# Kernel tuning notes

Hardware: AMD Instinct MI355X
Metric: run time of the kernel (lower is better)

## Reference

```python
import jax, jax.numpy as jnp
import numpy as np

SIGMA = 0.03   # self.sig = [0.03] in the original module
EPS = 1e-12    # guard for degenerate (zero-area) faces from random indices


def _mesh_quantities(V, F):
    """Face centers, areas (|0.5*cross|) and unit normals. V:[Nv,3], F:[Nf,3] int."""
    v0 = V[F[:, 0]]
    v1 = V[F[:, 1]]
    v2 = V[F[:, 2]]
    C = (v0 + v1 + v2) / 3.0                      # [Nf,3] face centers
    N = 0.5 * jnp.cross(v1 - v0, v2 - v0)         # [Nf,3] area-weighted normals
    L = jnp.linalg.norm(N, axis=-1)               # [Nf]  face areas
    Nn = N / jnp.maximum(L, EPS)[:, None]         # [Nf,3] unit normals
    return C, L, Nn


def _kernel_sum(Cx, Lx, Nx, Cy, Ly, Ny, gamma):
    """sum_ij Lx_i Ly_j exp(-gamma |Cx_i-Cy_j|^2) <Nx_i,Ny_j>^2  (unoriented Gauss-squared varifold kernel)."""
    d2 = (jnp.sum(Cx * Cx, -1)[:, None]
          + jnp.sum(Cy * Cy, -1)[None, :]
          - 2.0 * Cx @ Cy.T)                       # [F,F]
    dot = Nx @ Ny.T                                # [F,F]
    K = jnp.exp(-gamma * d2) * (dot * dot)
    return jnp.einsum('i,ij,j->', Lx, K, Ly)


def reference(predictions, targets, faces):
    gamma = 1.0 / (SIGMA * SIGMA)

    def per_sample(carry, xy):
        Vs, Vt = xy
        Cs, Ls, Ns = _mesh_quantities(Vs, faces)
        Ct, Lt, Nt = _mesh_quantities(Vt, faces)
        li = (_kernel_sum(Cs, Ls, Ns, Cs, Ls, Ns, gamma)
              + _kernel_sum(Ct, Lt, Nt, Ct, Lt, Nt, gamma)
              - 2.0 * _kernel_sum(Cs, Ls, Ns, Ct, Lt, Nt, gamma))
        return carry + li, None

    total, _ = jax.lax.scan(per_sample,
                            jnp.asarray(0.0, predictions.dtype),
                            (predictions, targets))
    return (total / predictions.shape[0])[None]   # shape [1], like torch.Tensor([0.0])


def setup_inputs() -> dict:
    key = jax.random.key(0)
    k1, k2, k3 = jax.random.split(key, 3)
    B, NV, NF = 4, 5023, 9976
    # scale 0.02 so inter-face distances are commensurate with sigma=0.03
    predictions = 0.02 * jax.random.normal(k1, (B, NV, 3), dtype=jnp.float32)
    targets = 0.02 * jax.random.normal(k2, (B, NV, 3), dtype=jnp.float32)
    faces = jax.random.randint(k3, (NF, 3), 0, NV, dtype=jnp.int32)
    return {"predictions": predictions, "targets": targets, "faces": faces}
```

## Files before the change

kernel.cpp:

```cpp
#include <hip/hip_runtime.h>


#define NVERT 5023
#define NFACE 9976
#define BATCH 4
#define HALFP 9984
#define NTP   (2 * HALFP)
#define NTOT  (BATCH * NTP)
#define NCH   624
#define NPAN  78
#define SPLITS 26

constexpr float GAMMA = 1.0f / (0.03f * 0.03f);
constexpr float LOG2E = 1.4426950408889634f;
constexpr float EPSV  = 1e-12f;

typedef _Float16 half8_t  __attribute__((ext_vector_type(8)));
typedef float    f32x16   __attribute__((ext_vector_type(16)));
typedef float    f32x2    __attribute__((ext_vector_type(2)));

__global__ __launch_bounds__(256)
void face_quant_kernel(const float* __restrict__ pred,
                       const float* __restrict__ targ,
                       const int*   __restrict__ faces,
                       _Float16*    __restrict__ fd,
                       float*       __restrict__ out) {
    int idx = blockIdx.x * 256 + threadIdx.x;
    if (idx == 0) out[0] = 0.0f;
    if (idx >= NTOT) return;

    int b     = idx / NTP;
    int s     = idx - b * NTP;
    int which = (s >= HALFP) ? 1 : 0;
    int f     = s - which * HALFP;

    _Float16* arec = fd + (size_t)idx * 32;
    _Float16* brec = fd + (size_t)NTOT * 32 + (size_t)idx * 32;

    if (f >= NFACE) {
        half8_t z = {};
        *(half8_t*)(arec + 0) = z; *(half8_t*)(arec + 8)  = z;
        *(half8_t*)(arec + 16) = z; *(half8_t*)(arec + 24) = z;
        *(half8_t*)(brec + 0) = z; *(half8_t*)(brec + 8)  = z;
        *(half8_t*)(brec + 16) = z; *(half8_t*)(brec + 24) = z;
        return;
    }

    const float* V = (which ? targ : pred) + (size_t)b * NVERT * 3;
    int i0 = faces[f * 3 + 0];
    int i1 = faces[f * 3 + 1];
    int i2 = faces[f * 3 + 2];

    float v0x = V[i0*3+0], v0y = V[i0*3+1], v0z = V[i0*3+2];
    float v1x = V[i1*3+0], v1y = V[i1*3+1], v1z = V[i1*3+2];
    float v2x = V[i2*3+0], v2y = V[i2*3+1], v2z = V[i2*3+2];

    const float third = 1.0f / 3.0f;
    float cx = (v0x + v1x + v2x) * third;
    float cy = (v0y + v1y + v2y) * third;
    float cz = (v0z + v1z + v2z) * third;

    float e1x = v1x - v0x, e1y = v1y - v0y, e1z = v1z - v0z;
    float e2x = v2x - v0x, e2y = v2y - v0y, e2z = v2z - v0z;

    float nx = 0.5f * (e1y * e2z - e1z * e2y);
    float ny = 0.5f * (e1z * e2x - e1x * e2z);
    float nz = 0.5f * (e1x * e2y - e1y * e2x);

    float L   = sqrtf(nx*nx + ny*ny + nz*nz);
    float inv = 1.0f / fmaxf(L, EPSV);
    float sc  = inv * sqrtf(L);
    float mx = nx * sc, my = ny * sc, mz = nz * sc;

    const float TG = 2.0f * GAMMA * LOG2E;
    float tgx = TG * cx, tgy = TG * cy, tgz = TG * cz;
    float cq  = -GAMMA * LOG2E * (cx*cx + cy*cy + cz*cz);

    _Float16 TGxh = (_Float16)tgx; _Float16 TGxl = (_Float16)(tgx - (float)TGxh);
    _Float16 TGyh = (_Float16)tgy; _Float16 TGyl = (_Float16)(tgy - (float)TGyh);
    _Float16 TGzh = (_Float16)tgz; _Float16 TGzl = (_Float16)(tgz - (float)TGzh);
    _Float16 Cxh  = (_Float16)cx;  _Float16 Cxl  = (_Float16)(cx  - (float)Cxh);
    _Float16 Cyh  = (_Float16)cy;  _Float16 Cyl  = (_Float16)(cy  - (float)Cyh);
    _Float16 Czh  = (_Float16)cz;  _Float16 Czl  = (_Float16)(cz  - (float)Czh);
    _Float16 cqh  = (_Float16)cq;  _Float16 cql  = (_Float16)(cq  - (float)cqh);
    _Float16 mxh  = (_Float16)mx;  _Float16 mxl  = (_Float16)(mx  - (float)mxh);
    _Float16 myh  = (_Float16)my;  _Float16 myl  = (_Float16)(my  - (float)myh);
    _Float16 mzh  = (_Float16)mz;  _Float16 mzl  = (_Float16)(mz  - (float)mzh);
    _Float16 one  = (_Float16)1.0f;
    _Float16 zz   = (_Float16)0.0f;

    half8_t ta0 = {TGxh, TGyh, TGzh, TGxl, TGyl, TGzl, TGxh, TGyh};
    half8_t ta1 = {TGzh, TGxl, TGyl, TGzl, cqh,  cql,  one,  one };
    half8_t da0 = {mxh,  myh,  mzh,  mxl,  myl,  mzl,  mxh,  myh };
    half8_t da1 = {mzh,  mxl,  myl,  mzl,  zz,   zz,   zz,   zz  };
    half8_t tb0 = {Cxh,  Cyh,  Czh,  Cxh,  Cyh,  Czh,  Cxl,  Cyl };
    half8_t tb1 = {Czl,  Cxl,  Cyl,  Czl,  one,  one,  cqh,  cql };
    half8_t db0 = {mxh,  myh,  mzh,  mxh,  myh,  mzh,  mxl,  myl };
    half8_t db1 = {mzl,  mxl,  myl,  mzl,  zz,   zz,   zz,   zz  };

    *(half8_t*)(arec + 0)  = ta0;  *(half8_t*)(arec + 8)  = ta1;
    *(half8_t*)(arec + 16) = da0;  *(half8_t*)(arec + 24) = da1;
    *(half8_t*)(brec + 0)  = tb0;  *(half8_t*)(brec + 8)  = tb1;
    *(half8_t*)(brec + 16) = db0;  *(half8_t*)(brec + 24) = db1;
}

__device__ __forceinline__ half8_t ld8(const _Float16* p) {
    return *(const half8_t*)p;
}

__global__ __launch_bounds__(256, 4)
void pair_sum_kernel(const _Float16* __restrict__ fd,
                     float*          __restrict__ out) {
    const int b       = blockIdx.z;
    const int pairIdx = blockIdx.x / SPLITS;
    const int s       = blockIdx.x % SPLITS;

    const _Float16* Arec = fd;
    const _Float16* Brec = fd + (size_t)NTOT * 32;

    const int lane = threadIdx.x & 63;
    const int w    = threadIdx.x >> 6;
    const int col  = lane & 31;
    const int koff = (lane >> 5) * 8;

    const size_t bface = (size_t)b * NTP;
    const size_t JSTEP = (size_t)SPLITS * 32 * 32;

    float acc = 0.0f;

    #pragma unroll 1
    for (int h = 0; h < 2; ++h) {
        const int   P  = h ? (NPAN - 1 - pairIdx) : pairIdx;
        const int   c0 = 8 * P;
        const float si = (P < NPAN / 2) ? 1.0f : -1.0f;
        const int   iters = (NCH - c0 - s + SPLITS - 1) / SPLITS;
        if (iters <= 0) continue;

        const _Float16* ap0 = Arec + (bface + (size_t)(P * 256 + w * 32 + col)) * 32 + koff;
        const _Float16* ap1 = ap0 + (size_t)128 * 32;
        half8_t aT0 = ld8(ap0);
        half8_t aD0 = ld8(ap0 + 16);
        half8_t aT1 = ld8(ap1);
        half8_t aD1 = ld8(ap1 + 16);

        const _Float16* pB = Brec + (bface + (size_t)((c0 + s) * 32 + col)) * 32 + koff;
        half8_t bT = ld8(pB);
        half8_t bD = ld8(pB + 16);

        f32x16 z = {};

        #pragma unroll 1
        for (int k = 0; k < iters; ++k) {
            const _Float16* pN = (k + 1 < iters) ? (pB + JSTEP) : pB;
            half8_t nT = ld8(pN);
            half8_t nD = ld8(pN + 16);
            pB = pN;

            f32x16 T0 = __builtin_amdgcn_mfma_f32_32x32x16_f16(aT0, bT, z, 0, 0, 0);
            f32x16 D0 = __builtin_amdgcn_mfma_f32_32x32x16_f16(aD0, bD, z, 0, 0, 0);
            f32x16 T1 = __builtin_amdgcn_mfma_f32_32x32x16_f16(aT1, bT, z, 0, 0, 0);
            f32x16 D1 = __builtin_amdgcn_mfma_f32_32x32x16_f16(aD1, bD, z, 0, 0, 0);

            f32x2 ts0 = {0.f, 0.f}, ts1 = {0.f, 0.f};
            #pragma unroll
            for (int r = 0; r < 16; r += 2) {
                f32x2 e0 = {__builtin_amdgcn_exp2f(T0[r]),
                            __builtin_amdgcn_exp2f(T0[r + 1])};
                f32x2 d0 = {D0[r], D0[r + 1]};
                d0 = d0 * d0;
                ts0 = e0 * d0 + ts0;
                f32x2 e1 = {__builtin_amdgcn_exp2f(T1[r]),
                            __builtin_amdgcn_exp2f(T1[r + 1])};
                f32x2 d1 = {D1[r], D1[r + 1]};
                d1 = d1 * d1;
                ts1 = e1 * d1 + ts1;
            }

            const int   jc  = c0 + s + SPLITS * k;
            const float sj  = (jc < NCH / 2) ? si : -si;
            const float wgt = (k == 0 && s < 8) ? 1.0f : 2.0f;
            acc = fmaf(sj * wgt, ts0.x + ts0.y + ts1.x + ts1.y, acc);

            bT = nT; bD = nD;
        }
    }

    acc *= (1.0f / BATCH);

    #pragma unroll
    for (int off = 32; off > 0; off >>= 1)
        acc += __shfl_down(acc, off, 64);

    __shared__ float wsum[4];
    if (lane == 0) wsum[w] = acc;
    __syncthreads();
    if (threadIdx.x == 0)
        atomicAdd(out, wsum[0] + wsum[1] + wsum[2] + wsum[3]);
}

extern "C" void kernel_launch(void* const* d_in, const int* in_sizes, int n_in,
                              void* d_out, int out_size, void* d_ws, size_t ws_size,
                              hipStream_t stream) {
    const float* pred  = (const float*)d_in[0];
    const float* targ  = (const float*)d_in[1];
    const int*   faces = (const int*)d_in[2];
    float*       out   = (float*)d_out;
    _Float16*    fd    = (_Float16*)d_ws;

    face_quant_kernel<<<(NTOT + 255) / 256, 256, 0, stream>>>(
        pred, targ, faces, fd, out);

    dim3 grid((NPAN / 2) * SPLITS, 1, BATCH);
    pair_sum_kernel<<<grid, 256, 0, stream>>>(fd, out);
}
```

Before: 157.2 us.

## Widen row panels to 512 faces and interleave MFMA with exp epilogue

Each block now covers 16 row chunks instead of 8, holding four A tiles in registers. Every streamed B tile therefore feeds four MFMA pairs, halving B loads per unit of work and halving the block count. Padding grows from 9984 to 10240 per half so panels divide evenly, which adds some wasted padded-pair work. The exp2 epilogues are interleaved between later MFMAs to hide matrix latency, at the cost of higher register pressure under the 4-blocks-per-CU launch bound.

```diff
diff --git a/kernel.cpp b/kernel.cpp
--- a/kernel.cpp
+++ b/kernel.cpp
@@ -4,11 +4,11 @@
 #define NVERT 5023
 #define NFACE 9976
 #define BATCH 4
-#define HALFP 9984
+#define HALFP 10240
 #define NTP   (2 * HALFP)
 #define NTOT  (BATCH * NTP)
-#define NCH   624
-#define NPAN  78
+#define NCH   640
+#define NPAN  40
 #define SPLITS 26
 
 constexpr float GAMMA = 1.0f / (0.03f * 0.03f);
@@ -131,23 +131,34 @@
     #pragma unroll 1
     for (int h = 0; h < 2; ++h) {
         const int   P  = h ? (NPAN - 1 - pairIdx) : pairIdx;
-        const int   c0 = 8 * P;
+        const int   c0 = 16 * P;
         const float si = (P < NPAN / 2) ? 1.0f : -1.0f;
         const int   iters = (NCH - c0 - s + SPLITS - 1) / SPLITS;
         if (iters <= 0) continue;
 
-        const _Float16* ap0 = Arec + (bface + (size_t)(P * 256 + w * 32 + col)) * 32 + koff;
-        const _Float16* ap1 = ap0 + (size_t)128 * 32;
-        half8_t aT0 = ld8(ap0);
-        half8_t aD0 = ld8(ap0 + 16);
-        half8_t aT1 = ld8(ap1);
-        half8_t aD1 = ld8(ap1 + 16);
+        const _Float16* ap0 = Arec + (bface + (size_t)(P * 512 + w * 32 + col)) * 32 + koff;
+        half8_t aT0 = ld8(ap0);                 half8_t aD0 = ld8(ap0 + 16);
+        half8_t aT1 = ld8(ap0 + 128 * 32);      half8_t aD1 = ld8(ap0 + 128 * 32 + 16);
+        half8_t aT2 = ld8(ap0 + 256 * 32);      half8_t aD2 = ld8(ap0 + 256 * 32 + 16);
+        half8_t aT3 = ld8(ap0 + 384 * 32);      half8_t aD3 = ld8(ap0 + 384 * 32 + 16);
 
         const _Float16* pB = Brec + (bface + (size_t)((c0 + s) * 32 + col)) * 32 + koff;
         half8_t bT = ld8(pB);
         half8_t bD = ld8(pB + 16);
 
         f32x16 z = {};
+
+        #define EPI(T_, D_, ts_)                                               \
+        {                                                                      \
+            _Pragma("unroll")                                                  \
+            for (int r = 0; r < 16; r += 2) {                                  \
+                f32x2 ee = {__builtin_amdgcn_exp2f((T_)[r]),                   \
+                            __builtin_amdgcn_exp2f((T_)[r + 1])};              \
+                f32x2 dd = {(D_)[r], (D_)[r + 1]};                             \
+                dd = dd * dd;                                                  \
+                ts_ = ee * dd + ts_;                                           \
+            }                                                                  \
+        }
 
         #pragma unroll 1
         for (int k = 0; k < iters; ++k) {
@@ -156,33 +167,29 @@
             half8_t nD = ld8(pN + 16);
             pB = pN;
 
+            f32x2 ts = {0.f, 0.f};
+
             f32x16 T0 = __builtin_amdgcn_mfma_f32_32x32x16_f16(aT0, bT, z, 0, 0, 0);
             f32x16 D0 = __builtin_amdgcn_mfma_f32_32x32x16_f16(aD0, bD, z, 0, 0, 0);
             f32x16 T1 = __builtin_amdgcn_mfma_f32_32x32x16_f16(aT1, bT, z, 0, 0, 0);
             f32x16 D1 = __builtin_amdgcn_mfma_f32_32x32x16_f16(aD1, bD, z, 0, 0, 0);
-
-            f32x2 ts0 = {0.f, 0.f}, ts1 = {0.f, 0.f};
-            #pragma unroll
-            for (int r = 0; r < 16; r += 2) {
-                f32x2 e0 = {__builtin_amdgcn_exp2f(T0[r]),
-                            __builtin_amdgcn_exp2f(T0[r + 1])};
-                f32x2 d0 = {D0[r], D0[r + 1]};
-                d0 = d0 * d0;
-                ts0 = e0 * d0 + ts0;
-                f32x2 e1 = {__builtin_amdgcn_exp2f(T1[r]),
-                            __builtin_amdgcn_exp2f(T1[r + 1])};
-                f32x2 d1 = {D1[r], D1[r + 1]};
-                d1 = d1 * d1;
-                ts1 = e1 * d1 + ts1;
-            }
+            EPI(T0, D0, ts);
+            f32x16 T2 = __builtin_amdgcn_mfma_f32_32x32x16_f16(aT2, bT, z, 0, 0, 0);
+            f32x16 D2 = __builtin_amdgcn_mfma_f32_32x32x16_f16(aD2, bD, z, 0, 0, 0);
+            EPI(T1, D1, ts);
+            f32x16 T3 = __builtin_amdgcn_mfma_f32_32x32x16_f16(aT3, bT, z, 0, 0, 0);
+            f32x16 D3 = __builtin_amdgcn_mfma_f32_32x32x16_f16(aD3, bD, z, 0, 0, 0);
+            EPI(T2, D2, ts);
+            EPI(T3, D3, ts);
 
             const int   jc  = c0 + s + SPLITS * k;
             const float sj  = (jc < NCH / 2) ? si : -si;
-            const float wgt = (k == 0 && s < 8) ? 1.0f : 2.0f;
-            acc = fmaf(sj * wgt, ts0.x + ts0.y + ts1.x + ts1.y, acc);
+            const float wgt = (k == 0 && s < 16) ? 1.0f : 2.0f;
+            acc = fmaf(sj * wgt, ts.x + ts.y, acc);
 
             bT = nT; bD = nD;
         }
+        #undef EPI
     }
 
     acc *= (1.0f / BATCH);
```

Result: slower. 176.0 us (+11.9%).
